# Performance work log

Measured on AMD Instinct MI355X. Metric: run time of the kernel, lower is better.

The kernel has to match this reference:

```python
import jax, jax.numpy as jnp
import numpy as np

N_SRC = 50000
N_DST = 50000
IN_FEATS = 256
OUT_FEATS = 32
NUM_HEADS = 4
N_EDGES = 800000


def setup_inputs() -> dict:
    key = jax.random.key(0)
    ks = jax.random.split(key, 7)
    h_src = jax.random.normal(ks[0], (N_SRC, IN_FEATS), dtype=jnp.float32)
    h_dst = jax.random.normal(ks[1], (N_DST, IN_FEATS), dtype=jnp.float32)
    # xavier-normal-ish scaling for the shared fc weight
    W = jax.random.normal(ks[2], (IN_FEATS, NUM_HEADS * OUT_FEATS), dtype=jnp.float32) * (
        jnp.sqrt(2.0) * jnp.sqrt(2.0 / (IN_FEATS + NUM_HEADS * OUT_FEATS))
    )
    attn_l = jax.random.normal(ks[3], (NUM_HEADS, OUT_FEATS), dtype=jnp.float32) * 0.1
    attn_r = jax.random.normal(ks[4], (NUM_HEADS, OUT_FEATS), dtype=jnp.float32) * 0.1
    src_idx = jax.random.randint(ks[5], (N_EDGES,), 0, N_SRC, dtype=jnp.int32)
    dst_idx = jax.random.randint(ks[6], (N_EDGES,), 0, N_DST, dtype=jnp.int32)
    return {"h_src": h_src, "h_dst": h_dst, "W": W, "attn_l": attn_l,
            "attn_r": attn_r, "src_idx": src_idx, "dst_idx": dst_idx}


def reference(h_src, h_dst, W, attn_l, attn_r, src_idx, dst_idx):
    H, F = NUM_HEADS, OUT_FEATS
    # shared linear projection (no bias), reshape to [N, H, F]
    ft_src = (h_src @ W).reshape(-1, H, F)            # [N_src, H, F]
    ft_dst = (h_dst @ W).reshape(-1, H, F)            # [N_dst, H, F]
    # per-node attention logits, [N, H]
    el = jnp.einsum('nhf,hf->nh', ft_src, attn_l)
    er = jnp.einsum('nhf,hf->nh', ft_dst, attn_r)
    # u_add_v gather over edges, LeakyReLU(0.2) -> [E, H]
    e = jax.nn.leaky_relu(el[src_idx] + er[dst_idx], negative_slope=0.2)
    # edge softmax over incoming edges of each destination node
    smax = jax.ops.segment_max(e, dst_idx, num_segments=N_DST)   # [N_dst, H]
    e_exp = jnp.exp(e - smax[dst_idx])                           # [E, H]
    ssum = jax.ops.segment_sum(e_exp, dst_idx, num_segments=N_DST)
    a = e_exp / ssum[dst_idx]                                    # [E, H]
    # u_mul_e + scatter-sum aggregation -> [N_dst, H, F]
    msg = ft_src[src_idx] * a[:, :, None]
    rst = jax.ops.segment_sum(msg, dst_idx, num_segments=N_DST)
    return rst
```

## Files before the change

kernel.cpp:

```cpp
#include <hip/hip_runtime.h>

#define IN_FEATS 256
#define OUT_FEATS 32
#define NUM_HEADS 4
#define NHF 128

typedef __attribute__((ext_vector_type(8))) short short8;
typedef __attribute__((ext_vector_type(4))) float f32x4;

__device__ inline unsigned short f2bf(float f) {
    unsigned int u = __builtin_bit_cast(unsigned int, f);
    u = (u + 0x7fff + ((u >> 16) & 1)) >> 16;
    return (unsigned short)u;
}
__device__ inline float bfhi2f(unsigned int packed_hi) {
    return __builtin_bit_cast(float, packed_hi);
}

__global__ __launch_bounds__(256) void prep_hist(const float* __restrict__ W,
                                                 const float* __restrict__ attn_r,
                                                 const int* __restrict__ dst,
                                                 float* __restrict__ v,
                                                 unsigned short* __restrict__ Wt,
                                                 int* __restrict__ partial,
                                                 int nb, int E) {
    const int t = threadIdx.x;
    const int b = blockIdx.x;
    if (b < 128) {
        Wt[b * 256 + t] = f2bf(W[(size_t)t * NHF + b]);
    } else if (b == 128) {
        for (int p = t; p < IN_FEATS * NUM_HEADS; p += 256) {
            int k = p >> 2, h = p & 3;
            const float* wr = W + (size_t)k * NHF + h * OUT_FEATS;
            const float* ar = attn_r + h * OUT_FEATS;
            float s = 0.f;
            #pragma unroll
            for (int f = 0; f < OUT_FEATS; ++f) s += wr[f] * ar[f];
            v[p] = s;
        }
    } else {
        __shared__ int cnt[256];
        const int hb = b - 129;
        const int chunk = (E + nb - 1) / nb;
        const int e0 = hb * chunk;
        const int e1 = min(e0 + chunk, E);
        cnt[t] = 0;
        __syncthreads();
        for (int e = e0 + t; e < e1; e += 256)
            atomicAdd(&cnt[dst[e] >> 8], 1);
        __syncthreads();
        partial[hb * 256 + t] = cnt[t];
    }
}

__global__ __launch_bounds__(256) void bin_pairs(const int* __restrict__ src,
                                                 const int* __restrict__ dst,
                                                 const int* __restrict__ partial,
                                                 unsigned int* __restrict__ pairs,
                                                 int nb, int E) {
    __shared__ int sc[256];
    __shared__ int basel[256];
    __shared__ int cnt[256];
    const int t = threadIdx.x;
    const int b = blockIdx.x;
    const int chunk = (E + nb - 1) / nb;
    const int e0 = b * chunk;
    const int e1 = min(e0 + chunk, E);

    int colsum = 0, rowpref = 0;
    for (int bb = 0; bb < nb; ++bb) {
        const int pv = partial[bb * 256 + t];
        colsum += pv;
        if (bb < b) rowpref += pv;
    }
    sc[t] = colsum;
    __syncthreads();
    #pragma unroll
    for (int d = 1; d < 256; d <<= 1) {
        int x = (t >= d) ? sc[t - d] : 0;
        __syncthreads();
        sc[t] += x;
        __syncthreads();
    }
    basel[t] = (sc[t] - colsum) + rowpref;
    cnt[t] = 0;
    __syncthreads();
    for (int e = e0 + t; e < e1; e += 256) {
        int d = dst[e];
        int bk = d >> 8;
        int o = atomicAdd(&cnt[bk], 1);
        pairs[basel[bk] + o] = (unsigned int)src[e] | ((unsigned int)(d & 255) << 16);
    }
}

__global__ __launch_bounds__(256) void compute_er(const float* __restrict__ hdst,
                                                  const float* __restrict__ v,
                                                  float* __restrict__ er, int M) {
    int wid  = (blockIdx.x * blockDim.x + threadIdx.x) >> 6;
    int lane = threadIdx.x & 63;
    if (wid >= M) return;
    const float4 x = *(const float4*)(hdst + (size_t)wid * IN_FEATS + lane * 4);
    const float4* vp = (const float4*)(v + (size_t)lane * 16);
    float4 v0 = vp[0], v1 = vp[1], v2 = vp[2], v3 = vp[3];
    float a0 = x.x * v0.x + x.y * v1.x + x.z * v2.x + x.w * v3.x;
    float a1 = x.x * v0.y + x.y * v1.y + x.z * v2.y + x.w * v3.y;
    float a2 = x.x * v0.z + x.y * v1.z + x.z * v2.z + x.w * v3.z;
    float a3 = x.x * v0.w + x.y * v1.w + x.z * v2.w + x.w * v3.w;
    #pragma unroll
    for (int m = 32; m >= 1; m >>= 1) {
        a0 += __shfl_xor(a0, m, 64);
        a1 += __shfl_xor(a1, m, 64);
        a2 += __shfl_xor(a2, m, 64);
        a3 += __shfl_xor(a3, m, 64);
    }
    if (lane == 0) *(float4*)(er + (size_t)wid * 4) = make_float4(a0, a1, a2, a3);
}

#define BSTRIDE 136
__global__ __launch_bounds__(256) void gemm_fine(const float* __restrict__ A,
                                                 const unsigned short* __restrict__ Wt,
                                                 const float* __restrict__ attn_l,
                                                 unsigned short* __restrict__ ft16,
                                                 float* __restrict__ el, int M,
                                                 const unsigned int* __restrict__ pairs,
                                                 const int* __restrict__ partial,
                                                 int* __restrict__ off,
                                                 int* __restrict__ csr_src,
                                                 int nb, int n_dst, int E) {
    __shared__ unsigned short WtL[128 * 256];

    if (blockIdx.x < (unsigned)nb) {
        int* cnt = (int*)WtL;
        int* cur = (int*)WtL + 256;
        int* sc  = (int*)WtL + 512;
        const int t = threadIdx.x;
        const int b = blockIdx.x;

        int colsum = 0;
        for (int bb = 0; bb < nb; ++bb) colsum += partial[bb * 256 + t];
        sc[t] = colsum;
        __syncthreads();
        #pragma unroll
        for (int d = 1; d < 256; d <<= 1) {
            int x = (t >= d) ? sc[t - d] : 0;
            __syncthreads();
            sc[t] += x;
            __syncthreads();
        }
        const int p1 = sc[b];
        const int p0 = (b == 0) ? 0 : sc[b - 1];

        cnt[t] = 0;
        __syncthreads();
        for (int p = p0 + t; p < p1; p += 256)
            atomicAdd(&cnt[pairs[p] >> 16], 1);
        __syncthreads();
        int vv = cnt[t];
        cur[t] = vv;
        __syncthreads();
        #pragma unroll
        for (int d = 1; d < 256; d <<= 1) {
            int x = (t >= d) ? cur[t - d] : 0;
            __syncthreads();
            cur[t] += x;
            __syncthreads();
        }
        int ex = cur[t] - vv;
        int node = b * 256 + t;
        if (node < n_dst) off[node] = p0 + ex;
        if (b == 0 && t == 0) off[n_dst] = E;
        __syncthreads();
        cur[t] = ex;
        __syncthreads();
        for (int p = p0 + t; p < p1; p += 256) {
            unsigned int pr = pairs[p];
            int o = atomicAdd(&cur[pr >> 16], 1);
            csr_src[p0 + o] = (int)(pr & 0xffffu);
        }
        return;
    }

    const int gb   = blockIdx.x - nb;
    const int wave = threadIdx.x >> 6;
    const int lane = threadIdx.x & 63;
    const int quad = lane >> 4;
    const int mc   = lane & 15;
    const int row_base = gb * 64 + wave * 16;

    for (int i = threadIdx.x; i < 4096; i += 256) {
        const int n = i >> 5, c = i & 31;
        const int cs = (c + n) & 31;
        *(uint4*)(WtL + n * 256 + cs * 8) = *(const uint4*)(Wt + n * 256 + c * 8);
    }

    float al[8];
    #pragma unroll
    for (int t = 0; t < 8; ++t) al[t] = attn_l[(t >> 1) * 32 + (t & 1) * 16 + mc];

    const int rowA = min(row_base + mc, M - 1);
    const float* arow = A + (size_t)rowA * IN_FEATS;

    float4 a[8][2];
    #pragma unroll
    for (int kk = 0; kk < 8; ++kk) {
        a[kk][0] = *(const float4*)(arow + kk * 32 + quad * 8);
        a[kk][1] = *(const float4*)(arow + kk * 32 + quad * 8 + 4);
    }

    f32x4 acc[8];
    #pragma unroll
    for (int t = 0; t < 8; ++t) acc[t] = (f32x4){0.f, 0.f, 0.f, 0.f};

    __syncthreads();

    #pragma unroll
    for (int kk = 0; kk < 8; ++kk) {
        short8 af;
        af[0] = (short)f2bf(a[kk][0].x); af[1] = (short)f2bf(a[kk][0].y);
        af[2] = (short)f2bf(a[kk][0].z); af[3] = (short)f2bf(a[kk][0].w);
        af[4] = (short)f2bf(a[kk][1].x); af[5] = (short)f2bf(a[kk][1].y);
        af[6] = (short)f2bf(a[kk][1].z); af[7] = (short)f2bf(a[kk][1].w);
        #pragma unroll
        for (int t = 0; t < 8; ++t) {
            const int n = t * 16 + mc;
            const int c = ((kk << 2) + quad + n) & 31;
            const short8 bf = *(const short8*)(WtL + n * 256 + c * 8);
            acc[t] = __builtin_amdgcn_mfma_f32_16x16x32_bf16(af, bf, acc[t], 0, 0, 0);
        }
    }

    float elp[4][4];
    #pragma unroll
    for (int v = 0; v < 4; ++v)
        #pragma unroll
        for (int h = 0; h < 4; ++h) elp[v][h] = 0.f;
    #pragma unroll
    for (int v = 0; v < 4; ++v)
        #pragma unroll
        for (int t = 0; t < 8; ++t) elp[v][t >> 1] += acc[t][v] * al[t];
    #pragma unroll
    for (int v = 0; v < 4; ++v)
        #pragma unroll
        for (int h = 0; h < 4; ++h) {
            #pragma unroll
            for (int d = 1; d < 16; d <<= 1)
                elp[v][h] += __shfl_xor(elp[v][h], d, 64);
        }

    #pragma unroll
    for (int v = 0; v < 4; ++v) {
        const int rg = row_base + quad * 4 + v;
        if (rg < M && mc < 4) {
            float ev = (mc == 0) ? elp[v][0] : (mc == 1) ? elp[v][1]
                     : (mc == 2) ? elp[v][2] : elp[v][3];
            el[(size_t)rg * 4 + mc] = ev;
        }
    }

    __syncthreads();
    #pragma unroll
    for (int v = 0; v < 4; ++v) {
        const int lr = wave * 16 + quad * 4 + v;
        #pragma unroll
        for (int t = 0; t < 8; ++t)
            WtL[lr * BSTRIDE + t * 16 + mc] = f2bf(acc[t][v]);
    }
    __syncthreads();
    const int rows_in_blk = min(64, M - gb * 64);
    for (int i = threadIdx.x; i < 64 * 16; i += 256) {
        const int lr = i >> 4, seg = i & 15;
        if (lr < rows_in_blk)
            *(uint4*)(ft16 + (size_t)(gb * 64 + lr) * NHF + seg * 8) =
                *(const uint4*)(WtL + lr * BSTRIDE + seg * 8);
    }
}

__global__ __launch_bounds__(256) void agg_pull(const int* __restrict__ off,
                                                const int* __restrict__ csr_src,
                                                const float* __restrict__ el,
                                                const float* __restrict__ er,
                                                const uint2* __restrict__ ftp,
                                                float* __restrict__ out, int n_dst) {
    const int wid  = (blockIdx.x * blockDim.x + threadIdx.x) >> 6;
    const int lane = threadIdx.x & 63;
    const int half = lane >> 5;
    const int hl   = lane & 31;
    const int node = wid * 2 + half;
    const bool valid = node < n_dst;
    const int nc = valid ? node : 0;
    const int h  = hl >> 3;
    const float er_h = er[nc * 4 + h];
    const int start = off[nc];
    const int end   = valid ? off[nc + 1] : start;
    const int deg   = end - start;
    const int last  = max(end - 1, 0);

    const int sl = csr_src[min(start + hl, last)];

    const int mdeg  = max(deg, __shfl_xor(deg, 32, 64));
    const int iters = (min(mdeg, 32) + 7) >> 3;

    float a0 = 0.f, a1 = 0.f, a2 = 0.f, a3 = 0.f, sw = 0.f;

    float e[8]; uint2 q[8];
    #pragma unroll
    for (int j = 0; j < 8; ++j) {
        const int s = __shfl(sl, j, 32);
        e[j] = el[s * 4 + h];
        q[j] = ftp[s * 32 + hl];
    }

    for (int i = 0; i < iters; ++i) {
        float f[8]; uint2 r[8];
        const int jn = (i + 1) << 3;
        #pragma unroll
        for (int j = 0; j < 8; ++j) {
            const int s = __shfl(sl, min(jn + j, 31), 32);
            f[j] = el[s * 4 + h];
            r[j] = ftp[s * 32 + hl];
        }

        const int kb = start + (i << 3);
        #pragma unroll
        for (int j = 0; j < 8; ++j) {
            float x = e[j] + er_h;
            x = fmaxf(x, 0.2f * x);
            const float w = (kb + j < end) ? __expf(x) : 0.f;
            sw += w;
            a0 = fmaf(bfhi2f(q[j].x << 16),          w, a0);
            a1 = fmaf(bfhi2f(q[j].x & 0xffff0000u),  w, a1);
            a2 = fmaf(bfhi2f(q[j].y << 16),          w, a2);
            a3 = fmaf(bfhi2f(q[j].y & 0xffff0000u),  w, a3);
        }

        #pragma unroll
        for (int j = 0; j < 8; ++j) { e[j] = f[j]; q[j] = r[j]; }
    }

    for (int k = start + 32; k < end; ++k) {
        const int s = csr_src[k];
        float x = el[s * 4 + h] + er_h;
        x = fmaxf(x, 0.2f * x);
        const float w = __expf(x);
        const uint2 qq = ftp[s * 32 + hl];
        sw += w;
        a0 = fmaf(bfhi2f(qq.x << 16),         w, a0);
        a1 = fmaf(bfhi2f(qq.x & 0xffff0000u), w, a1);
        a2 = fmaf(bfhi2f(qq.y << 16),         w, a2);
        a3 = fmaf(bfhi2f(qq.y & 0xffff0000u), w, a3);
    }

    if (valid) {
        const float inv = (deg > 0) ? 1.f / sw : 0.f;
        float4 r;
        r.x = a0 * inv; r.y = a1 * inv; r.z = a2 * inv; r.w = a3 * inv;
        *(float4*)(out + (size_t)node * NHF + hl * 4) = r;
    }
}

extern "C" void kernel_launch(void* const* d_in, const int* in_sizes, int n_in,
                              void* d_out, int out_size, void* d_ws, size_t ws_size,
                              hipStream_t stream) {
    const float* h_src  = (const float*)d_in[0];
    const float* h_dst  = (const float*)d_in[1];
    const float* W      = (const float*)d_in[2];
    const float* attn_l = (const float*)d_in[3];
    const float* attn_r = (const float*)d_in[4];
    const int* src_idx  = (const int*)d_in[5];
    const int* dst_idx  = (const int*)d_in[6];

    const int n_src = in_sizes[0] / IN_FEATS;
    const int n_dst = in_sizes[1] / IN_FEATS;
    const int E     = in_sizes[5];

    const int nb = (n_dst + 255) >> 8;

    char* ws = (char*)d_ws;
    size_t o = 0;
    float* v       = (float*)(ws + o); o += 4096;
    float* el      = (float*)(ws + o); o += (size_t)n_src * 4 * sizeof(float);
    float* er      = (float*)(ws + o); o += (size_t)n_dst * 4 * sizeof(float);
    int*   off     = (int*)(ws + o);   o += ((size_t)n_dst + 16) * sizeof(int);
    int*   partial = (int*)(ws + o);   o += 256 * 256 * sizeof(int);
    unsigned short* Wt = (unsigned short*)(ws + o); o += (size_t)NHF * IN_FEATS * sizeof(unsigned short);
    int*   csr_src = (int*)(ws + o);   o += (size_t)E * sizeof(int);
    unsigned int* pairs = (unsigned int*)(ws + o); o += (size_t)E * sizeof(unsigned int);
    unsigned short* ft16 = (unsigned short*)(ws + o); o += (size_t)n_src * NHF * sizeof(unsigned short);

    float* out = (float*)d_out;

    prep_hist<<<129 + nb, 256, 0, stream>>>(W, attn_r, dst_idx, v, Wt, partial, nb, E);
    bin_pairs<<<nb, 256, 0, stream>>>(src_idx, dst_idx, partial, pairs, nb, E);
    compute_er<<<(n_dst + 3) / 4, 256, 0, stream>>>(h_dst, v, er, n_dst);
    gemm_fine<<<nb + (n_src + 63) / 64, 256, 0, stream>>>(h_src, Wt, attn_l, ft16, el,
                                                          n_src, pairs, partial, off,
                                                          csr_src, nb, n_dst, E);
    {
        const int nwave = (n_dst + 1) >> 1;
        agg_pull<<<(nwave + 3) / 4, 256, 0, stream>>>(off, csr_src, el, er,
                                                      (const uint2*)ft16, out, n_dst);
    }
}
```

Measured before the change: 258.1 us.

## Move fine CSR binning into er kernel and precompute bucket bases

Result: no change. 256.3 us (-0.7%).

```diff
diff --git a/kernel.cpp b/kernel.cpp
--- a/kernel.cpp
+++ b/kernel.cpp
@@ -57,6 +57,7 @@
                                                  const int* __restrict__ dst,
                                                  const int* __restrict__ partial,
                                                  unsigned int* __restrict__ pairs,
+                                                 int* __restrict__ bbase,
                                                  int nb, int E) {
     __shared__ int sc[256];
     __shared__ int basel[256];
@@ -82,6 +83,10 @@
         sc[t] += x;
         __syncthreads();
     }
+    if (b == 0) {
+        bbase[t] = sc[t] - colsum;
+        if (t == 255) bbase[256] = sc[255];
+    }
     basel[t] = (sc[t] - colsum) + rowpref;
     cnt[t] = 0;
     __syncthreads();
@@ -93,10 +98,52 @@
     }
 }
 
-__global__ __launch_bounds__(256) void compute_er(const float* __restrict__ hdst,
-                                                  const float* __restrict__ v,
-                                                  float* __restrict__ er, int M) {
-    int wid  = (blockIdx.x * blockDim.x + threadIdx.x) >> 6;
+__global__ __launch_bounds__(256) void er_fine(const float* __restrict__ hdst,
+                                               const float* __restrict__ v,
+                                               float* __restrict__ er, int M,
+                                               const unsigned int* __restrict__ pairs,
+                                               const int* __restrict__ bbase,
+                                               int* __restrict__ off,
+                                               int* __restrict__ csr_src,
+                                               int nb, int n_dst, int E) {
+    __shared__ int cnt[256];
+    __shared__ int cur[256];
+
+    if (blockIdx.x < (unsigned)nb) {
+        const int t = threadIdx.x;
+        const int b = blockIdx.x;
+        const int p0 = bbase[b], p1 = bbase[b + 1];
+        cnt[t] = 0;
+        __syncthreads();
+        for (int p = p0 + t; p < p1; p += 256)
+            atomicAdd(&cnt[pairs[p] >> 16], 1);
+        __syncthreads();
+        int vv = cnt[t];
+        cur[t] = vv;
+        __syncthreads();
+        #pragma unroll
+        for (int d = 1; d < 256; d <<= 1) {
+            int x = (t >= d) ? cur[t - d] : 0;
+            __syncthreads();
+            cur[t] += x;
+            __syncthreads();
+        }
+        int ex = cur[t] - vv;
+        int node = b * 256 + t;
+        if (node < n_dst) off[node] = p0 + ex;
+        if (b == 0 && t == 0) off[n_dst] = E;
+        __syncthreads();
+        cur[t] = ex;
+        __syncthreads();
+        for (int p = p0 + t; p < p1; p += 256) {
+            unsigned int pr = pairs[p];
+            int o = atomicAdd(&cur[pr >> 16], 1);
+            csr_src[p0 + o] = (int)(pr & 0xffffu);
+        }
+        return;
+    }
+
+    int wid  = ((blockIdx.x - nb) * 256 + threadIdx.x) >> 6;
     int lane = threadIdx.x & 63;
     if (wid >= M) return;
     const float4 x = *(const float4*)(hdst + (size_t)wid * IN_FEATS + lane * 4);
@@ -117,75 +164,18 @@
 }
 
 #define BSTRIDE 136
-__global__ __launch_bounds__(256) void gemm_fine(const float* __restrict__ A,
-                                                 const unsigned short* __restrict__ Wt,
-                                                 const float* __restrict__ attn_l,
-                                                 unsigned short* __restrict__ ft16,
-                                                 float* __restrict__ el, int M,
-                                                 const unsigned int* __restrict__ pairs,
-                                                 const int* __restrict__ partial,
-                                                 int* __restrict__ off,
-                                                 int* __restrict__ csr_src,
-                                                 int nb, int n_dst, int E) {
+__global__ __launch_bounds__(256) void gemm_el(const float* __restrict__ A,
+                                               const unsigned short* __restrict__ Wt,
+                                               const float* __restrict__ attn_l,
+                                               unsigned short* __restrict__ ft16,
+                                               float* __restrict__ el, int M) {
     __shared__ unsigned short WtL[128 * 256];
 
-    if (blockIdx.x < (unsigned)nb) {
-        int* cnt = (int*)WtL;
-        int* cur = (int*)WtL + 256;
-        int* sc  = (int*)WtL + 512;
-        const int t = threadIdx.x;
-        const int b = blockIdx.x;
-
-        int colsum = 0;
-        for (int bb = 0; bb < nb; ++bb) colsum += partial[bb * 256 + t];
-        sc[t] = colsum;
-        __syncthreads();
-        #pragma unroll
-        for (int d = 1; d < 256; d <<= 1) {
-            int x = (t >= d) ? sc[t - d] : 0;
-            __syncthreads();
-            sc[t] += x;
-            __syncthreads();
-        }
-        const int p1 = sc[b];
-        const int p0 = (b == 0) ? 0 : sc[b - 1];
-
-        cnt[t] = 0;
-        __syncthreads();
-        for (int p = p0 + t; p < p1; p += 256)
-            atomicAdd(&cnt[pairs[p] >> 16], 1);
-        __syncthreads();
-        int vv = cnt[t];
-        cur[t] = vv;
-        __syncthreads();
-        #pragma unroll
-        for (int d = 1; d < 256; d <<= 1) {
-            int x = (t >= d) ? cur[t - d] : 0;
-            __syncthreads();
-            cur[t] += x;
-            __syncthreads();
-        }
-        int ex = cur[t] - vv;
-        int node = b * 256 + t;
-        if (node < n_dst) off[node] = p0 + ex;
-        if (b == 0 && t == 0) off[n_dst] = E;
-        __syncthreads();
-        cur[t] = ex;
-        __syncthreads();
-        for (int p = p0 + t; p < p1; p += 256) {
-            unsigned int pr = pairs[p];
-            int o = atomicAdd(&cur[pr >> 16], 1);
-            csr_src[p0 + o] = (int)(pr & 0xffffu);
-        }
-        return;
-    }
-
-    const int gb   = blockIdx.x - nb;
     const int wave = threadIdx.x >> 6;
     const int lane = threadIdx.x & 63;
     const int quad = lane >> 4;
     const int mc   = lane & 15;
-    const int row_base = gb * 64 + wave * 16;
+    const int row_base = blockIdx.x * 64 + wave * 16;
 
     for (int i = threadIdx.x; i < 4096; i += 256) {
         const int n = i >> 5, c = i & 31;
@@ -266,11 +256,11 @@
             WtL[lr * BSTRIDE + t * 16 + mc] = f2bf(acc[t][v]);
     }
     __syncthreads();
-    const int rows_in_blk = min(64, M - gb * 64);
+    const int rows_in_blk = min(64, M - blockIdx.x * 64);
     for (int i = threadIdx.x; i < 64 * 16; i += 256) {
         const int lr = i >> 4, seg = i & 15;
         if (lr < rows_in_blk)
-            *(uint4*)(ft16 + (size_t)(gb * 64 + lr) * NHF + seg * 8) =
+            *(uint4*)(ft16 + (size_t)(blockIdx.x * 64 + lr) * NHF + seg * 8) =
                 *(const uint4*)(WtL + lr * BSTRIDE + seg * 8);
     }
 }
@@ -381,6 +371,7 @@
     float* el      = (float*)(ws + o); o += (size_t)n_src * 4 * sizeof(float);
     float* er      = (float*)(ws + o); o += (size_t)n_dst * 4 * sizeof(float);
     int*   off     = (int*)(ws + o);   o += ((size_t)n_dst + 16) * sizeof(int);
+    int*   bbase   = (int*)(ws + o);   o += 260 * sizeof(int);
     int*   partial = (int*)(ws + o);   o += 256 * 256 * sizeof(int);
     unsigned short* Wt = (unsigned short*)(ws + o); o += (size_t)NHF * IN_FEATS * sizeof(unsigned short);
     int*   csr_src = (int*)(ws + o);   o += (size_t)E * sizeof(int);
@@ -390,11 +381,13 @@
     float* out = (float*)d_out;
 
     prep_hist<<<129 + nb, 256, 0, stream>>>(W, attn_r, dst_idx, v, Wt, partial, nb, E);
-    bin_pairs<<<nb, 256, 0, stream>>>(src_idx, dst_idx, partial, pairs, nb, E);
-    compute_er<<<(n_dst + 3) / 4, 256, 0, stream>>>(h_dst, v, er, n_dst);
-    gemm_fine<<<nb + (n_src + 63) / 64, 256, 0, stream>>>(h_src, Wt, attn_l, ft16, el,
-                                                          n_src, pairs, partial, off,
-                                                          csr_src, nb, n_dst, E);
+    bin_pairs<<<nb, 256, 0, stream>>>(src_idx, dst_idx, partial, pairs, bbase, nb, E);
+    gemm_el<<<(n_src + 63) / 64, 256, 0, stream>>>(h_src, Wt, attn_l, ft16, el, n_src);
+    {
+        const int er_blocks = (n_src > 0) ? ((n_dst * 64 + 255) / 256) : 0;
+        er_fine<<<nb + er_blocks, 256, 0, stream>>>(h_dst, v, er, n_dst, pairs,
+                                                    bbase, off, csr_src, nb, n_dst, E);
+    }
     {
         const int nwave = (n_dst + 1) >> 1;
         agg_pull<<<(nwave + 3) / 4, 256, 0, stream>>>(off, csr_src, el, er,
```
